# Kernel tuning notes

Measured on AMD Instinct MI355X. Metric: run time of the kernel, lower is better.

The kernel has to match this reference:

```python
import jax, jax.numpy as jnp
import numpy as np

B, S, D, H, FF = 4, 2048, 512, 8, 2048
HD = D // H
WINDOW = 64  # local attention half-window in rank space
EPS = 1e-5


def _layer_norm(v, g, b):
    m = jnp.mean(v, axis=-1, keepdims=True)
    var = jnp.mean(jnp.square(v - m), axis=-1, keepdims=True)
    return (v - m) / jnp.sqrt(var + EPS) * g + b


def setup_inputs() -> dict:
    key = jax.random.key(0)
    ks = jax.random.split(key, 10)
    sc = 0.02
    x = jax.random.normal(ks[0], (B, S, D), jnp.float32)
    padding_mask = jnp.zeros((B, S), dtype=bool)
    i = jnp.arange(S)
    local = jnp.abs(i[:, None] - i[None, :]) <= WINDOW
    glob = (i[:, None] == 0) | (i[None, :] == 0)  # global spectrum token at pos 0
    attn_mask = jnp.where(local | glob, 0.0, -jnp.inf).astype(jnp.float32)
    return {
        "x": x,
        "padding_mask": padding_mask,
        "attn_mask": attn_mask,
        "in_proj_w": jax.random.normal(ks[1], (3 * D, D), jnp.float32) * sc,
        "in_proj_b": jnp.zeros((3 * D,), jnp.float32),
        "out_proj_w": jax.random.normal(ks[2], (D, D), jnp.float32) * sc,
        "out_proj_b": jnp.zeros((D,), jnp.float32),
        "ln1_g": jnp.ones((D,), jnp.float32),
        "ln1_b": jnp.zeros((D,), jnp.float32),
        "ln2_g": jnp.ones((D,), jnp.float32),
        "ln2_b": jnp.zeros((D,), jnp.float32),
        "ff_w1": jax.random.normal(ks[3], (FF, D), jnp.float32) * sc,
        "ff_b1": jnp.zeros((FF,), jnp.float32),
        "ff_w2": jax.random.normal(ks[4], (D, FF), jnp.float32) * sc,
        "ff_b2": jnp.zeros((D,), jnp.float32),
    }


def reference(x, padding_mask, attn_mask, in_proj_w, in_proj_b, out_proj_w,
              out_proj_b, ln1_g, ln1_b, ln2_g, ln2_b, ff_w1, ff_b1, ff_w2, ff_b2):
    # pre-LN attention
    a = _layer_norm(x, ln1_g, ln1_b)
    qkv = a @ in_proj_w.T + in_proj_b  # [B,S,3D]
    q, k, v = jnp.split(qkv, 3, axis=-1)
    to_heads = lambda t: t.reshape(B, S, H, HD).transpose(0, 2, 1, 3)
    q, k, v = to_heads(q), to_heads(k), to_heads(v)
    scores = jnp.einsum('bhqd,bhkd->bhqk', q, k) * (HD ** -0.5)
    # float attn_mask path: key_padding_mask converted to additive -inf floats
    kpm = jnp.where(padding_mask, -jnp.inf, 0.0).astype(scores.dtype)
    scores = scores + attn_mask[None, None, :, :] + kpm[:, None, None, :]
    p = jax.nn.softmax(scores, axis=-1)
    o = jnp.einsum('bhqk,bhkd->bhqd', p, v).transpose(0, 2, 1, 3).reshape(B, S, D)
    o = o @ out_proj_w.T + out_proj_b
    x = x + o  # residual (dropout = 0)
    # pre-LN feed-forward with exact GELU (torch nn.GELU default)
    f = _layer_norm(x, ln2_g, ln2_b)
    f = jax.nn.gelu(f @ ff_w1.T + ff_b1, approximate=False) @ ff_w2.T + ff_b2
    return x + f
```

## Files before the change

### kernel.cpp

```cpp
#include <hip/hip_runtime.h>
#include <hip/hip_bf16.h>
#include <math.h>

namespace {

constexpr int kB = 4, kS = 2048, kD = 512, kH = 8, kFF = 2048;
constexpr int kM = kB * kS;
constexpr int kHD = kD / kH;
constexpr int kWin = 64;

typedef __attribute__((ext_vector_type(8))) short short8;
typedef __attribute__((ext_vector_type(4))) float f32x4;

__device__ __forceinline__ float bf2f(__hip_bfloat16 v) { return __bfloat162float(v); }
__device__ __forceinline__ __hip_bfloat16 f2bf(float v) { return __float2bfloat16(v); }
__device__ __forceinline__ int iclamp(int v, int lo, int hi) { return v < lo ? lo : (v > hi ? hi : v); }

__global__ void cast_f32_bf16(const float* __restrict__ s, __hip_bfloat16* __restrict__ d, int n) {
  int i = (blockIdx.x * blockDim.x + threadIdx.x) * 4;
  if (i >= n) return;
  float4 v = *(const float4*)(s + i);
  union { __hip_bfloat16 h[4]; uint2 u; } t;
  t.h[0] = f2bf(v.x); t.h[1] = f2bf(v.y); t.h[2] = f2bf(v.z); t.h[3] = f2bf(v.w);
  *(uint2*)(d + i) = t.u;
}

__global__ __launch_bounds__(64)
void ln_rows(const float* __restrict__ x, const float* __restrict__ g,
             const float* __restrict__ bta, __hip_bfloat16* __restrict__ out) {
  int row = blockIdx.x;
  int lane = threadIdx.x;
  const float* xr = x + (size_t)row * kD;
  int c = lane * 8;
  float4 v0 = *(const float4*)(xr + c);
  float4 v1 = *(const float4*)(xr + c + 4);
  float s  = v0.x + v0.y + v0.z + v0.w + v1.x + v1.y + v1.z + v1.w;
  float ss = v0.x*v0.x + v0.y*v0.y + v0.z*v0.z + v0.w*v0.w
           + v1.x*v1.x + v1.y*v1.y + v1.z*v1.z + v1.w*v1.w;
#pragma unroll
  for (int o = 32; o > 0; o >>= 1) { s += __shfl_xor(s, o); ss += __shfl_xor(ss, o); }
  float mean = s * (1.0f / kD);
  float inv  = rsqrtf(ss * (1.0f / kD) - mean * mean + 1e-5f);
  float4 g0 = *(const float4*)(g + c),   g1 = *(const float4*)(g + c + 4);
  float4 b0 = *(const float4*)(bta + c), b1 = *(const float4*)(bta + c + 4);
  union { __hip_bfloat16 h[8]; int4 u; } t;
  t.h[0] = f2bf((v0.x - mean) * inv * g0.x + b0.x);
  t.h[1] = f2bf((v0.y - mean) * inv * g0.y + b0.y);
  t.h[2] = f2bf((v0.z - mean) * inv * g0.z + b0.z);
  t.h[3] = f2bf((v0.w - mean) * inv * g0.w + b0.w);
  t.h[4] = f2bf((v1.x - mean) * inv * g1.x + b1.x);
  t.h[5] = f2bf((v1.y - mean) * inv * g1.y + b1.y);
  t.h[6] = f2bf((v1.z - mean) * inv * g1.z + b1.z);
  t.h[7] = f2bf((v1.w - mean) * inv * g1.w + b1.w);
  *(int4*)(out + (size_t)row * kD + c) = t.u;
}

__global__ __launch_bounds__(64)
void attn_tile(const __hip_bfloat16* __restrict__ qkv, __hip_bfloat16* __restrict__ o) {
  const int bh = blockIdx.x;
  const int tq = blockIdx.y;
  const int b = bh >> 3, h = bh & 7;
  const int lane = threadIdx.x;
  const int quad = lane >> 4, col = lane & 15;
  const int q0 = tq * 16;
  const int kbase = q0 - kWin;

  __shared__ __hip_bfloat16 Pt[160 * 20];

  const __hip_bfloat16* base = qkv + (size_t)b * kS * (3 * kD);

  short8 aq0, aq1;
  {
    const __hip_bfloat16* qrow = base + (size_t)(q0 + col) * (3 * kD) + h * kHD + quad * 8;
    aq0 = *(const short8*)qrow;
    aq1 = *(const short8*)(qrow + 32);
  }

  f32x4 sc[10];
#pragma unroll
  for (int t = 0; t < 10; ++t) {
    int krow = (t < 9) ? iclamp(kbase + t * 16 + col, 0, kS - 1) : col;
    const short8* kp = (const short8*)(base + (size_t)krow * (3 * kD) + kD + h * kHD + quad * 8);
    f32x4 a = (f32x4){0.f, 0.f, 0.f, 0.f};
    a = __builtin_amdgcn_mfma_f32_16x16x32_bf16(aq0, kp[0], a, 0, 0, 0);
    a = __builtin_amdgcn_mfma_f32_16x16x32_bf16(aq1, kp[4], a, 0, 0, 0);
    sc[t] = a;
  }

  float rowmax[4] = {-1e30f, -1e30f, -1e30f, -1e30f};
#pragma unroll
  for (int t = 0; t < 10; ++t) {
#pragma unroll
    for (int r = 0; r < 4; ++r) {
      int q = q0 + quad * 4 + r;
      bool valid;
      if (t < 9) {
        int k = kbase + t * 16 + col;
        valid = (k >= 0) && (k < kS) && ((q - k <= kWin && k - q <= kWin) || k == 0);
      } else {
        valid = (col == 0) && (kbase > 0);
      }
      float s = valid ? sc[t][r] * 0.125f : -1e30f;
      sc[t][r] = s;
      rowmax[r] = fmaxf(rowmax[r], s);
    }
  }
#pragma unroll
  for (int r = 0; r < 4; ++r)
#pragma unroll
    for (int off = 1; off < 16; off <<= 1)
      rowmax[r] = fmaxf(rowmax[r], __shfl_xor(rowmax[r], off));

  float rowsum[4] = {0.f, 0.f, 0.f, 0.f};
#pragma unroll
  for (int t = 0; t < 10; ++t)
#pragma unroll
    for (int r = 0; r < 4; ++r) {
      float e = __expf(sc[t][r] - rowmax[r]);
      sc[t][r] = e;
      rowsum[r] += e;
    }
#pragma unroll
  for (int r = 0; r < 4; ++r)
#pragma unroll
    for (int off = 1; off < 16; off <<= 1)
      rowsum[r] += __shfl_xor(rowsum[r], off);

#pragma unroll
  for (int t = 0; t < 10; ++t) {
    union { ushort u[4]; unsigned long long ll; } pk;
#pragma unroll
    for (int r = 0; r < 4; ++r) {
      __hip_bfloat16 hv = f2bf(sc[t][r]);
      pk.u[r] = *(ushort*)&hv;
    }
    *(unsigned long long*)&Pt[(t * 16 + col) * 20 + quad * 4] = pk.ll;
  }
  __syncthreads();

  f32x4 oacc[4];
#pragma unroll
  for (int n = 0; n < 4; ++n) oacc[n] = (f32x4){0.f, 0.f, 0.f, 0.f};

#pragma unroll
  for (int c = 0; c < 5; ++c) {
    union { short s[8]; short8 v; } pa;
    const __hip_bfloat16* vrow[8];
#pragma unroll
    for (int j = 0; j < 8; ++j) {
      int kidx = c * 32 + quad * 8 + j;
      pa.s[j] = *(const short*)&Pt[kidx * 20 + col];
      int key = (kidx < 144) ? iclamp(kbase + kidx, 0, kS - 1) : (kidx - 144);
      vrow[j] = base + (size_t)key * (3 * kD) + 2 * kD + h * kHD;
    }
#pragma unroll
    for (int n = 0; n < 4; ++n) {
      union { short s[8]; short8 v; } vb;
#pragma unroll
      for (int j = 0; j < 8; ++j) vb.s[j] = *(const short*)(vrow[j] + n * 16 + col);
      oacc[n] = __builtin_amdgcn_mfma_f32_16x16x32_bf16(pa.v, vb.v, oacc[n], 0, 0, 0);
    }
  }

#pragma unroll
  for (int n = 0; n < 4; ++n)
#pragma unroll
    for (int r = 0; r < 4; ++r) {
      int q = q0 + quad * 4 + r;
      o[(size_t)(b * kS + q) * kD + h * kHD + n * 16 + col] = f2bf(oacc[n][r] / rowsum[r]);
    }
}

__global__ __launch_bounds__(1024)
void attn_q0(const __hip_bfloat16* __restrict__ qkv, __hip_bfloat16* __restrict__ o) {
  const int b = blockIdx.x >> 3, h = blockIdx.x & 7;
  const int t = threadIdx.x;
  const int lane = t & 63, wid = t >> 6;
  __shared__ float qs[kHD];
  __shared__ float sc[kS];
  __shared__ float redm[16];
  __shared__ float reds[16];
  __shared__ float part[16][kHD];

  const __hip_bfloat16* base = qkv + (size_t)b * kS * (3 * kD);
  if (t < kHD) qs[t] = bf2f(base[h * kHD + t]) * 0.125f;
  __syncthreads();

  float m = -1e30f;
#pragma unroll
  for (int it = 0; it < 2; ++it) {
    int k = t + it * 1024;
    const short8* kp = (const short8*)(base + (size_t)k * (3 * kD) + kD + h * kHD);
    float s = 0.f;
#pragma unroll
    for (int cc = 0; cc < 8; ++cc) {
      union { short8 v; __hip_bfloat16 hh[8]; } u;
      u.v = kp[cc];
#pragma unroll
      for (int d = 0; d < 8; ++d) s += qs[cc * 8 + d] * bf2f(u.hh[d]);
    }
    sc[k] = s;
    m = fmaxf(m, s);
  }
#pragma unroll
  for (int off = 32; off > 0; off >>= 1) m = fmaxf(m, __shfl_xor(m, off));
  if (lane == 0) redm[wid] = m;
  __syncthreads();
  float M = redm[0];
#pragma unroll
  for (int i = 1; i < 16; ++i) M = fmaxf(M, redm[i]);

  float ls = 0.f;
#pragma unroll
  for (int it = 0; it < 2; ++it) {
    int k = t + it * 1024;
    float e = __expf(sc[k] - M);
    sc[k] = e;
    ls += e;
  }
#pragma unroll
  for (int off = 32; off > 0; off >>= 1) ls += __shfl_xor(ls, off);
  if (lane == 0) reds[wid] = ls;
  __syncthreads();
  float L = 0.f;
#pragma unroll
  for (int i = 0; i < 16; ++i) L += reds[i];

  float a = 0.f;
  const int d = lane;
#pragma unroll 8
  for (int kk = 0; kk < 128; ++kk) {
    int k = wid * 128 + kk;
    a += sc[k] * bf2f(base[(size_t)k * (3 * kD) + 2 * kD + h * kHD + d]);
  }
  part[wid][d] = a;
  __syncthreads();
  if (t < kHD) {
    float s = 0.f;
#pragma unroll
    for (int c = 0; c < 16; ++c) s += part[c][t];
    o[(size_t)(b * kS) * kD + h * kHD + t] = f2bf(s / L);
  }
}

template <int EPI, typename OT>
__global__ __launch_bounds__(256, 2)
void gemm_bt(const __hip_bfloat16* __restrict__ A, const __hip_bfloat16* __restrict__ W,
             const float* __restrict__ bias, const float* __restrict__ resid,
             OT* __restrict__ C, int Ndim, int K) {
  __shared__ __hip_bfloat16 As[128][72];
  __shared__ __hip_bfloat16 Ws[128][72];

  const int tid = threadIdx.x;
  const int lane = tid & 63, w = tid >> 6;
  const int wm = w >> 1, wn = w & 1;
  const int quad = lane >> 4, mrow = lane & 15;
  const int m0 = blockIdx.y * 128, n0 = blockIdx.x * 128;

  f32x4 acc[4][4];
#pragma unroll
  for (int i = 0; i < 4; ++i)
#pragma unroll
    for (int j = 0; j < 4; ++j) acc[i][j] = (f32x4){0.f, 0.f, 0.f, 0.f};

  for (int kt = 0; kt < K; kt += 64) {
#pragma unroll
    for (int it = 0; it < 4; ++it) {
      int idx = it * 256 + tid;
      int r = idx >> 3, cc = (idx & 7) << 3;
      *(int4*)&As[r][cc] = *(const int4*)(A + (size_t)(m0 + r) * K + kt + cc);
      *(int4*)&Ws[r][cc] = *(const int4*)(W + (size_t)(n0 + r) * K + kt + cc);
    }
    __syncthreads();
#pragma unroll
    for (int kk = 0; kk < 64; kk += 32) {
      int kb = kk + quad * 8;
      short8 af[4], bf[4];
#pragma unroll
      for (int i = 0; i < 4; ++i) af[i] = *(const short8*)&As[wm * 64 + i * 16 + mrow][kb];
#pragma unroll
      for (int j = 0; j < 4; ++j) bf[j] = *(const short8*)&Ws[wn * 64 + j * 16 + mrow][kb];
#pragma unroll
      for (int i = 0; i < 4; ++i)
#pragma unroll
        for (int j = 0; j < 4; ++j)
          acc[i][j] = __builtin_amdgcn_mfma_f32_16x16x32_bf16(af[i], bf[j], acc[i][j], 0, 0, 0);
    }
    __syncthreads();
  }

#pragma unroll
  for (int i = 0; i < 4; ++i) {
#pragma unroll
    for (int r = 0; r < 4; ++r) {
      int row = m0 + wm * 64 + i * 16 + quad * 4 + r;
#pragma unroll
      for (int j = 0; j < 4; ++j) {
        int col = n0 + wn * 64 + j * 16 + mrow;
        float v = acc[i][j][r] + bias[col];
        if (EPI == 1) v = 0.5f * v * (1.0f + erff(v * 0.70710678118f));
        if (EPI == 2) v += resid[(size_t)row * Ndim + col];
        if constexpr (__is_same(OT, float)) C[(size_t)row * Ndim + col] = v;
        else                                C[(size_t)row * Ndim + col] = f2bf(v);
      }
    }
  }
}

}

extern "C" void kernel_launch(void* const* d_in, const int* in_sizes, int n_in,
                              void* d_out, int out_size, void* d_ws, size_t ws_size,
                              hipStream_t stream) {
  const float* x          = (const float*)d_in[0];
  const float* in_proj_w  = (const float*)d_in[3];
  const float* in_proj_b  = (const float*)d_in[4];
  const float* out_proj_w = (const float*)d_in[5];
  const float* out_proj_b = (const float*)d_in[6];
  const float* ln1_g      = (const float*)d_in[7];
  const float* ln1_b      = (const float*)d_in[8];
  const float* ln2_g      = (const float*)d_in[9];
  const float* ln2_b      = (const float*)d_in[10];
  const float* ff_w1      = (const float*)d_in[11];
  const float* ff_b1      = (const float*)d_in[12];
  const float* ff_w2      = (const float*)d_in[13];
  const float* ff_b2      = (const float*)d_in[14];
  float* out = (float*)d_out;

  char* ws = (char*)d_ws;
  size_t off = 0;
  auto carve = [&](size_t bytes) { char* p = ws + off; off += (bytes + 255) & ~(size_t)255; return p; };
  __hip_bfloat16* wqkv_bf = (__hip_bfloat16*)carve((size_t)3 * kD * kD * 2);
  __hip_bfloat16* wout_bf = (__hip_bfloat16*)carve((size_t)kD * kD * 2);
  __hip_bfloat16* wff1_bf = (__hip_bfloat16*)carve((size_t)kFF * kD * 2);
  __hip_bfloat16* wff2_bf = (__hip_bfloat16*)carve((size_t)kD * kFF * 2);
  __hip_bfloat16* a_bf    = (__hip_bfloat16*)carve((size_t)kM * kD * 2);
  __hip_bfloat16* qkv_bf  = (__hip_bfloat16*)carve((size_t)kM * 3 * kD * 2);
  __hip_bfloat16* o_bf    = (__hip_bfloat16*)carve((size_t)kM * kD * 2);
  float*          r1      = (float*)carve((size_t)kM * kD * 4);
  __hip_bfloat16* ln2_bf  = (__hip_bfloat16*)carve((size_t)kM * kD * 2);
  __hip_bfloat16* ff1_bf  = (__hip_bfloat16*)carve((size_t)kM * kFF * 2);

  {
    int n;
    n = 3 * kD * kD; cast_f32_bf16<<<(n / 4 + 255) / 256, 256, 0, stream>>>(in_proj_w, wqkv_bf, n);
    n = kD * kD;     cast_f32_bf16<<<(n / 4 + 255) / 256, 256, 0, stream>>>(out_proj_w, wout_bf, n);
    n = kFF * kD;    cast_f32_bf16<<<(n / 4 + 255) / 256, 256, 0, stream>>>(ff_w1, wff1_bf, n);
    n = kD * kFF;    cast_f32_bf16<<<(n / 4 + 255) / 256, 256, 0, stream>>>(ff_w2, wff2_bf, n);
  }

  ln_rows<<<kM, 64, 0, stream>>>(x, ln1_g, ln1_b, a_bf);
  gemm_bt<0, __hip_bfloat16><<<dim3(1536 / 128, kM / 128), 256, 0, stream>>>(
      a_bf, wqkv_bf, in_proj_b, nullptr, qkv_bf, 3 * kD, kD);
  attn_tile<<<dim3(kB * kH, kS / 16), 64, 0, stream>>>(qkv_bf, o_bf);
  attn_q0<<<kB * kH, 1024, 0, stream>>>(qkv_bf, o_bf);
  gemm_bt<2, float><<<dim3(kD / 128, kM / 128), 256, 0, stream>>>(
      o_bf, wout_bf, out_proj_b, x, r1, kD, kD);
  ln_rows<<<kM, 64, 0, stream>>>(r1, ln2_g, ln2_b, ln2_bf);
  gemm_bt<1, __hip_bfloat16><<<dim3(kFF / 128, kM / 128), 256, 0, stream>>>(
      ln2_bf, wff1_bf, ff_b1, nullptr, ff1_bf, kFF, kD);
  gemm_bt<2, float><<<dim3(kD / 128, kM / 128), 256, 0, stream>>>(
      ff1_bf, wff2_bf, ff_b2, r1, out, kD, kFF);
}
```

Baseline: 273.8 us.

## Use direct global-to-LDS loads with XOR swizzle and narrower tiles for N=512 GEMMs

The GEMM now loads A and W tiles with global_load_lds 16-byte async copies straight into shared memory, skipping the register round trip. LDS uses an XOR-swizzled unpadded layout so fragment reads avoid bank conflicts. A TN template parameter lets the two N=512 GEMMs use 64-wide tiles, doubling their block count for better CU occupancy. The async loads still sit behind a single __syncthreads with no double buffering, and correctness depends on each wave writing exactly a contiguous 512-element chunk matching the swizzle.

```diff
diff --git a/kernel.cpp b/kernel.cpp
--- a/kernel.cpp
+++ b/kernel.cpp
@@ -15,6 +15,11 @@
 __device__ __forceinline__ float bf2f(__hip_bfloat16 v) { return __bfloat162float(v); }
 __device__ __forceinline__ __hip_bfloat16 f2bf(float v) { return __float2bfloat16(v); }
 __device__ __forceinline__ int iclamp(int v, int lo, int hi) { return v < lo ? lo : (v > hi ? hi : v); }
+
+__device__ __forceinline__ void async16(const void* g, void* l) {
+  __builtin_amdgcn_global_load_lds((const __attribute__((address_space(1))) void*)g,
+                                   (__attribute__((address_space(3))) void*)l, 16, 0, 0);
+}
 
 __global__ void cast_f32_bf16(const float* __restrict__ s, __hip_bfloat16* __restrict__ d, int n) {
   int i = (blockIdx.x * blockDim.x + threadIdx.x) * 4;
@@ -243,48 +248,58 @@
   }
 }
 
-template <int EPI, typename OT>
+template <int TN, int EPI, typename OT>
 __global__ __launch_bounds__(256, 2)
 void gemm_bt(const __hip_bfloat16* __restrict__ A, const __hip_bfloat16* __restrict__ W,
              const float* __restrict__ bias, const float* __restrict__ resid,
              OT* __restrict__ C, int Ndim, int K) {
-  __shared__ __hip_bfloat16 As[128][72];
-  __shared__ __hip_bfloat16 Ws[128][72];
+  constexpr int NF = TN / 32;
+  __shared__ __hip_bfloat16 As[128 * 64];
+  __shared__ __hip_bfloat16 Ws[TN * 64];
 
   const int tid = threadIdx.x;
   const int lane = tid & 63, w = tid >> 6;
   const int wm = w >> 1, wn = w & 1;
   const int quad = lane >> 4, mrow = lane & 15;
-  const int m0 = blockIdx.y * 128, n0 = blockIdx.x * 128;
-
-  f32x4 acc[4][4];
+  const int m0 = blockIdx.y * 128, n0 = blockIdx.x * TN;
+
+  const int lrow = lane >> 3;
+  const int lcol = ((lane & 7) ^ lrow) << 3;
+
+  f32x4 acc[4][NF];
 #pragma unroll
   for (int i = 0; i < 4; ++i)
 #pragma unroll
-    for (int j = 0; j < 4; ++j) acc[i][j] = (f32x4){0.f, 0.f, 0.f, 0.f};
+    for (int j = 0; j < NF; ++j) acc[i][j] = (f32x4){0.f, 0.f, 0.f, 0.f};
 
   for (int kt = 0; kt < K; kt += 64) {
 #pragma unroll
     for (int it = 0; it < 4; ++it) {
-      int idx = it * 256 + tid;
-      int r = idx >> 3, cc = (idx & 7) << 3;
-      *(int4*)&As[r][cc] = *(const int4*)(A + (size_t)(m0 + r) * K + kt + cc);
-      *(int4*)&Ws[r][cc] = *(const int4*)(W + (size_t)(n0 + r) * K + kt + cc);
+      int c = w * 4 + it;
+      async16(A + (size_t)(m0 + c * 8 + lrow) * K + kt + lcol, &As[c * 512]);
+    }
+#pragma unroll
+    for (int it = 0; it < NF; ++it) {
+      int c = w * NF + it;
+      async16(W + (size_t)(n0 + c * 8 + lrow) * K + kt + lcol, &Ws[c * 512]);
     }
     __syncthreads();
 #pragma unroll
     for (int kk = 0; kk < 64; kk += 32) {
-      int kb = kk + quad * 8;
-      short8 af[4], bf[4];
-#pragma unroll
-      for (int i = 0; i < 4; ++i) af[i] = *(const short8*)&As[wm * 64 + i * 16 + mrow][kb];
-#pragma unroll
-      for (int j = 0; j < 4; ++j) bf[j] = *(const short8*)&Ws[wn * 64 + j * 16 + mrow][kb];
+      const int ch = (kk >> 3) + quad;
+      const int sw = (ch ^ (mrow & 7)) << 3;
+      short8 af[4], wf[NF];
 #pragma unroll
       for (int i = 0; i < 4; ++i)
-#pragma unroll
-        for (int j = 0; j < 4; ++j)
-          acc[i][j] = __builtin_amdgcn_mfma_f32_16x16x32_bf16(af[i], bf[j], acc[i][j], 0, 0, 0);
+        af[i] = *(const short8*)&As[(wm * 64 + i * 16 + mrow) * 64 + sw];
+#pragma unroll
+      for (int j = 0; j < NF; ++j)
+        wf[j] = *(const short8*)&Ws[(wn * (TN / 2) + j * 16 + mrow) * 64 + sw];
+#pragma unroll
+      for (int i = 0; i < 4; ++i)
+#pragma unroll
+        for (int j = 0; j < NF; ++j)
+          acc[i][j] = __builtin_amdgcn_mfma_f32_16x16x32_bf16(af[i], wf[j], acc[i][j], 0, 0, 0);
     }
     __syncthreads();
   }
@@ -295,8 +310,8 @@
     for (int r = 0; r < 4; ++r) {
       int row = m0 + wm * 64 + i * 16 + quad * 4 + r;
 #pragma unroll
-      for (int j = 0; j < 4; ++j) {
-        int col = n0 + wn * 64 + j * 16 + mrow;
+      for (int j = 0; j < NF; ++j) {
+        int col = n0 + wn * (TN / 2) + j * 16 + mrow;
         float v = acc[i][j][r] + bias[col];
         if (EPI == 1) v = 0.5f * v * (1.0f + erff(v * 0.70710678118f));
         if (EPI == 2) v += resid[(size_t)row * Ndim + col];
@@ -350,15 +365,15 @@
   }
 
   ln_rows<<<kM, 64, 0, stream>>>(x, ln1_g, ln1_b, a_bf);
-  gemm_bt<0, __hip_bfloat16><<<dim3(1536 / 128, kM / 128), 256, 0, stream>>>(
+  gemm_bt<128, 0, __hip_bfloat16><<<dim3(1536 / 128, kM / 128), 256, 0, stream>>>(
       a_bf, wqkv_bf, in_proj_b, nullptr, qkv_bf, 3 * kD, kD);
   attn_tile<<<dim3(kB * kH, kS / 16), 64, 0, stream>>>(qkv_bf, o_bf);
   attn_q0<<<kB * kH, 1024, 0, stream>>>(qkv_bf, o_bf);
-  gemm_bt<2, float><<<dim3(kD / 128, kM / 128), 256, 0, stream>>>(
+  gemm_bt<64, 2, float><<<dim3(kD / 64, kM / 128), 256, 0, stream>>>(
       o_bf, wout_bf, out_proj_b, x, r1, kD, kD);
   ln_rows<<<kM, 64, 0, stream>>>(r1, ln2_g, ln2_b, ln2_bf);
-  gemm_bt<1, __hip_bfloat16><<<dim3(kFF / 128, kM / 128), 256, 0, stream>>>(
+  gemm_bt<128, 1, __hip_bfloat16><<<dim3(kFF / 128, kM / 128), 256, 0, stream>>>(
       ln2_bf, wff1_bf, ff_b1, nullptr, ff1_bf, kFF, kD);
-  gemm_bt<2, float><<<dim3(kD / 128, kM / 128), 256, 0, stream>>>(
+  gemm_bt<64, 2, float><<<dim3(kD / 64, kM / 128), 256, 0, stream>>>(
       ff1_bf, wff2_bf, ff_b2, r1, out, kD, kFF);
 }
```

Result: faster. 267.5 us (-2.3%).
